# Performance work log

Measured on AMD Instinct MI355X. Metric: run time of the kernel, lower is better.

## Reference

```python
import jax, jax.numpy as jnp
import numpy as np

DIM = 1024
HEADS = 16
HEAD_DIM = DIM // HEADS
B, N = 512, 65
EPS = 1e-5


def layernorm(x, w, b):
    # LayerNorm over last dim (head_dim), eps matching torch default
    mu = jnp.mean(x, axis=-1, keepdims=True)
    var = jnp.var(x, axis=-1, keepdims=True)
    return (x - mu) * jax.lax.rsqrt(var + EPS) * w + b


def setup_inputs() -> dict:
    key = jax.random.key(0)
    ks = jax.random.split(key, 8)
    s = 0.02
    return {
        "x": jax.random.normal(ks[0], (B, N, DIM), dtype=jnp.float32),
        "w_qkv": jax.random.normal(ks[1], (3 * DIM, DIM), dtype=jnp.float32) * s,
        "w_proj": jax.random.normal(ks[2], (DIM, DIM), dtype=jnp.float32) * s,
        "qn_w": jnp.ones((HEAD_DIM,), jnp.float32),
        "qn_b": jnp.zeros((HEAD_DIM,), jnp.float32),
        "kn_w": jnp.ones((HEAD_DIM,), jnp.float32),
        "kn_b": jnp.zeros((HEAD_DIM,), jnp.float32),
        "bias": jax.random.normal(ks[3], (HEADS, 65, 65), dtype=jnp.float32) * 0.1,
        "bias_scale": jnp.array(1.0, jnp.float32),
    }


def reference(x, w_qkv, w_proj, qn_w, qn_b, kn_w, kn_b, bias, bias_scale):
    Bsz, n, C = x.shape
    scale = HEAD_DIM ** -0.5
    qkv = jnp.einsum('bnc,dc->bnd', x, w_qkv)              # [B,N,3C]
    qkv = qkv.reshape(Bsz, n, 3, HEADS, HEAD_DIM)
    qkv = jnp.transpose(qkv, (2, 0, 3, 1, 4))              # [3,B,H,N,hd]
    q, k, v = qkv[0], qkv[1], qkv[2]
    q = layernorm(q, qn_w, qn_b) * scale
    k = layernorm(k, kn_w, kn_b)
    attn = jnp.einsum('bhnd,bhmd->bhnm', q, k)             # [B,H,N,N]
    attn = attn + (bias[:, :n, :n] * bias_scale)[None]
    attn = jax.nn.softmax(attn, axis=-1)
    out = jnp.einsum('bhnm,bhmd->bhnd', attn, v)           # [B,H,N,hd]
    out = jnp.transpose(out, (0, 2, 1, 3)).reshape(Bsz, n, C)
    return jnp.einsum('bnc,dc->bnd', out, w_proj)
```

## Files before the change

kernel.cpp:

```cpp
#include <hip/hip_runtime.h>
#include <stdint.h>

#define HEADS 16
#define BSZ 512
#define NTOK 65
#define MTOK (BSZ * NTOK)
#define NX  34078720UL
#define NQW 3145728UL
#define NPW 1048576UL

typedef __attribute__((ext_vector_type(8))) short bf16x8;
typedef __attribute__((ext_vector_type(4))) float f32x4;

__device__ __forceinline__ unsigned short f2bf(float f) {
  unsigned u = __float_as_uint(f);
  u += 0x7FFFu + ((u >> 16) & 1u);
  return (unsigned short)(u >> 16);
}

__global__ __launch_bounds__(256) void cast3_kernel(
    const float* __restrict__ x, const float* __restrict__ wq, const float* __restrict__ wp,
    unsigned short* __restrict__ xb, unsigned short* __restrict__ wqb, unsigned short* __restrict__ wpb) {
  size_t u = ((size_t)blockIdx.x * 256 + threadIdx.x) * 4;
  const float* src; unsigned short* dst; size_t off;
  if (u < NX)            { src = x;  dst = xb;  off = u; }
  else if (u < NX + NQW) { src = wq; dst = wqb; off = u - NX; }
  else                   { src = wp; dst = wpb; off = u - NX - NQW; }
  float4 v = *(const float4*)(src + off);
  ushort4 o;
  o.x = f2bf(v.x); o.y = f2bf(v.y); o.z = f2bf(v.z); o.w = f2bf(v.w);
  *(ushort4*)(dst + off) = o;
}

__global__ __launch_bounds__(512, 2) void gemm0_256_kernel(
    const unsigned short* __restrict__ A, const unsigned short* __restrict__ Bm,
    unsigned short* __restrict__ qws, unsigned short* __restrict__ kws,
    unsigned short* __restrict__ vws,
    const float* __restrict__ qn_w, const float* __restrict__ qn_b,
    const float* __restrict__ kn_w, const float* __restrict__ kn_b) {
  __shared__ unsigned short As0[256 * 64];
  __shared__ unsigned short Bs0[256 * 64];
  __shared__ unsigned short As1[256 * 64];
  __shared__ unsigned short Bs1[256 * 64];
  const int tid = threadIdx.x;
  const int wid = tid >> 6, lane = tid & 63;
  const int lrow = lane & 15, lk = lane >> 4;
  const int wm = wid >> 2, wn = wid & 3;

  const int orig = blockIdx.x;
  const int wg = (orig & 7) * 195 + (orig >> 3);
  const int bm = wg / 12, bn = wg - bm * 12;

  const size_t arow0 = (size_t)bm * 256, brow0 = (size_t)bn * 256;

  const unsigned short* pA[4];
  const unsigned short* pB[4];
  int dstc[4];
#pragma unroll
  for (int j = 0; j < 4; ++j) {
    int ci = j * 512 + tid;
    int row = ci >> 3;
    int k8 = (ci & 7) ^ (row & 7);
    pA[j] = A + (arow0 + row) * 1024 + k8 * 8;
    pB[j] = Bm + (brow0 + row) * 1024 + k8 * 8;
    dstc[j] = (j * 512 + wid * 64) * 4;
  }

  f32x4 acc[2][4][4] = {};

  auto stage = [&](unsigned short* __restrict__ dA, unsigned short* __restrict__ dB, int ktn) {
    const int koff = ktn * 64;
#pragma unroll
    for (int j = 0; j < 4; ++j) {
      __builtin_amdgcn_global_load_lds(
          (const __attribute__((address_space(1))) unsigned int*)(pA[j] + koff),
          (__attribute__((address_space(3))) unsigned int*)dA + dstc[j], 16, 0, 0);
      __builtin_amdgcn_global_load_lds(
          (const __attribute__((address_space(1))) unsigned int*)(pB[j] + koff),
          (__attribute__((address_space(3))) unsigned int*)dB + dstc[j], 16, 0, 0);
    }
  };

  auto ktile = [&](const unsigned short* __restrict__ RA, const unsigned short* __restrict__ RB,
                   unsigned short* __restrict__ WA, unsigned short* __restrict__ WB, int ktn) {
    if (ktn < 16) stage(WA, WB, ktn);
#pragma unroll
    for (int kk = 0; kk < 2; ++kk) {
      const int cpos8 = ((kk * 4 + lk) ^ (lrow & 7)) * 8;
      bf16x8 bv[4];
#pragma unroll
      for (int nt = 0; nt < 4; ++nt)
        bv[nt] = *(const bf16x8*)&RB[(wn * 64 + nt * 16 + lrow) * 64 + cpos8];
#pragma unroll
      for (int mh = 0; mh < 2; ++mh) {
        bf16x8 av[4];
#pragma unroll
        for (int mt = 0; mt < 4; ++mt)
          av[mt] = *(const bf16x8*)&RA[(wm * 128 + mh * 64 + mt * 16 + lrow) * 64 + cpos8];
        __builtin_amdgcn_s_barrier();
        __builtin_amdgcn_s_setprio(1);
#pragma unroll
        for (int mt = 0; mt < 4; ++mt)
#pragma unroll
          for (int nt = 0; nt < 4; ++nt)
            acc[mh][mt][nt] =
                __builtin_amdgcn_mfma_f32_16x16x32_bf16(av[mt], bv[nt], acc[mh][mt][nt], 0, 0, 0);
        __builtin_amdgcn_s_setprio(0);
      }
    }
    __syncthreads();
  };

  stage(As0, Bs0, 0);
  __syncthreads();

#pragma unroll 1
  for (int kt2 = 0; kt2 < 8; ++kt2) {
    ktile(As0, Bs0, As1, Bs1, 2 * kt2 + 1);
    ktile(As1, Bs1, As0, Bs0, 2 * kt2 + 2);
  }

  const int sec = bn >> 2;
  const int h0 = ((bn & 3) << 2) + wn;
  const float qsc = (sec == 0) ? 0.125f : 1.0f;
  float wv[4], bvv[4];
  if (sec < 2) {
    const float* wp_ = sec ? kn_w : qn_w;
    const float* bp_ = sec ? kn_b : qn_b;
#pragma unroll
    for (int nt = 0; nt < 4; ++nt) {
      wv[nt] = wp_[nt * 16 + lrow];
      bvv[nt] = bp_[nt * 16 + lrow];
    }
  }
  unsigned short* qk_dst = sec ? kws : qws;
#pragma unroll
  for (int mh = 0; mh < 2; ++mh)
#pragma unroll
    for (int mt = 0; mt < 4; ++mt)
#pragma unroll
      for (int r = 0; r < 4; ++r) {
        int grow = bm * 256 + wm * 128 + mh * 64 + mt * 16 + lk * 4 + r;
        int b = grow / 65, nn = grow - b * 65;
        int bh = b * HEADS + h0;
        if (sec < 2) {
          float s = 0.f, s2 = 0.f;
#pragma unroll
          for (int nt = 0; nt < 4; ++nt) {
            float f = acc[mh][mt][nt][r];
            s += f; s2 += f * f;
          }
          s += __shfl_xor(s, 1); s2 += __shfl_xor(s2, 1);
          s += __shfl_xor(s, 2); s2 += __shfl_xor(s2, 2);
          s += __shfl_xor(s, 4); s2 += __shfl_xor(s2, 4);
          s += __shfl_xor(s, 8); s2 += __shfl_xor(s2, 8);
          float mu = s * 0.015625f;
          float rstd = rsqrtf(s2 * 0.015625f - mu * mu + 1e-5f);
          size_t base = ((size_t)bh * 65 + nn) * 64;
#pragma unroll
          for (int nt = 0; nt < 4; ++nt)
            qk_dst[base + nt * 16 + lrow] =
                f2bf(((acc[mh][mt][nt][r] - mu) * rstd * wv[nt] + bvv[nt]) * qsc);
        } else {
#pragma unroll
          for (int nt = 0; nt < 4; ++nt)
            vws[((size_t)bh * 64 + nt * 16 + lrow) * 80 + nn] = f2bf(acc[mh][mt][nt][r]);
        }
      }
}

template <int MODE>
__global__ __launch_bounds__(256) void gemm_bt_kernel(
    const unsigned short* __restrict__ A, const unsigned short* __restrict__ Bm,
    unsigned short* __restrict__ qws, unsigned short* __restrict__ kws,
    unsigned short* __restrict__ vws, float* __restrict__ outp,
    const float* __restrict__ qn_w, const float* __restrict__ qn_b,
    const float* __restrict__ kn_w, const float* __restrict__ kn_b) {
  __shared__ unsigned short As[128 * 64];
  __shared__ unsigned short Bs[128 * 64];
  const int tid = threadIdx.x;
  const int wid = tid >> 6, lane = tid & 63;
  const int lrow = lane & 15, lk = lane >> 4;
  const int bm = blockIdx.y, bn = blockIdx.x;
  const int wr = (wid >> 1) * 64, wc = (wid & 1) * 64;
  const size_t arow0 = (size_t)bm * 128, brow0 = (size_t)bn * 128;

  f32x4 acc[4][4] = {};

  for (int kt = 0; kt < 16; ++kt) {
    __syncthreads();
    const int k0 = kt * 64;
#pragma unroll
    for (int j = 0; j < 4; ++j) {
      int ci = j * 256 + tid;
      int row = ci >> 3, k8s = ci & 7;
      int k8 = k8s ^ (row & 7);
      const unsigned short* srcA = A + (arow0 + row) * 1024 + k0 + k8 * 8;
      __builtin_amdgcn_global_load_lds(
          (const __attribute__((address_space(1))) unsigned int*)srcA,
          (__attribute__((address_space(3))) unsigned int*)As + (size_t)(j * 256 + wid * 64) * 4,
          16, 0, 0);
      const unsigned short* srcB = Bm + (brow0 + row) * 1024 + k0 + k8 * 8;
      __builtin_amdgcn_global_load_lds(
          (const __attribute__((address_space(1))) unsigned int*)srcB,
          (__attribute__((address_space(3))) unsigned int*)Bs + (size_t)(j * 256 + wid * 64) * 4,
          16, 0, 0);
    }
    __syncthreads();
#pragma unroll
    for (int kk = 0; kk < 2; ++kk) {
      const int cpos = (kk * 4 + lk) ^ (lrow & 7);
      bf16x8 af[4], bfv[4];
#pragma unroll
      for (int mt = 0; mt < 4; ++mt)
        af[mt] = *(const bf16x8*)&As[(wr + mt * 16 + lrow) * 64 + cpos * 8];
#pragma unroll
      for (int nt = 0; nt < 4; ++nt)
        bfv[nt] = *(const bf16x8*)&Bs[(wc + nt * 16 + lrow) * 64 + cpos * 8];
#pragma unroll
      for (int mt = 0; mt < 4; ++mt)
#pragma unroll
        for (int nt = 0; nt < 4; ++nt)
          acc[mt][nt] = __builtin_amdgcn_mfma_f32_16x16x32_bf16(af[mt], bfv[nt], acc[mt][nt], 0, 0, 0);
    }
  }

  if (MODE == 0) {
  } else {
    const size_t cb = (size_t)bn * 128 + wc + lrow;
#pragma unroll
    for (int mt = 0; mt < 4; ++mt)
#pragma unroll
      for (int r = 0; r < 4; ++r) {
        float* rp = outp + (size_t)(bm * 128 + wr + mt * 16 + lk * 4 + r) * 1024 + cb;
#pragma unroll
        for (int nt = 0; nt < 4; ++nt) rp[nt * 16] = acc[mt][nt][r];
      }
  }
}

__global__ __launch_bounds__(256, 4) void attn_kernel(
    const unsigned short* __restrict__ qws, const unsigned short* __restrict__ kws,
    const unsigned short* __restrict__ vws,
    const float* __restrict__ bias, const float* __restrict__ bias_scale,
    unsigned short* __restrict__ aws) {
  __shared__ unsigned short qk_s[2 * 80 * 64];
  __shared__ unsigned short v_s[64 * 128];
  const int tid = threadIdx.x;
  const int wid = tid >> 6;
  const int bh = blockIdx.x;
  const int b = bh >> 4, h = bh & 15;
  const size_t qbase = (size_t)bh * 65 * 64;
  const size_t vbase = (size_t)bh * 64 * 80;

#pragma unroll
  for (int it = 0; it < 2; ++it) {
    int ci = it * 256 + tid;
    int row = ci >> 3, k8s = ci & 7;
    int k8 = k8s ^ (row & 7);
    __builtin_amdgcn_global_load_lds(
        (const __attribute__((address_space(1))) unsigned int*)(qws + qbase + row * 64 + k8 * 8),
        (__attribute__((address_space(3))) unsigned int*)qk_s + (size_t)(it * 256 + wid * 64) * 4,
        16, 0, 0);
    __builtin_amdgcn_global_load_lds(
        (const __attribute__((address_space(1))) unsigned int*)(kws + qbase + row * 64 + k8 * 8),
        (__attribute__((address_space(3))) unsigned int*)qk_s + (size_t)(640 + it * 256 + wid * 64) * 4,
        16, 0, 0);
  }
  if (tid < 8) {
    bf16x8 tq = *(const bf16x8*)&qws[qbase + 64 * 64 + tid * 8];
    *(bf16x8*)&qk_s[64 * 64 + tid * 8] = tq;
  } else if (tid < 16) {
    int t = tid - 8;
    bf16x8 tk = *(const bf16x8*)&kws[qbase + 64 * 64 + t * 8];
    *(bf16x8*)&qk_s[5120 + 64 * 64 + t * 8] = tk;
  }
#pragma unroll
  for (int it = 0; it < 4; ++it) {
    int ci = it * 256 + tid;
    int d = ci >> 4, cs = ci & 15;
    int c = cs ^ (d & 7);
    __builtin_amdgcn_global_load_lds(
        (const __attribute__((address_space(1))) unsigned int*)(vws + vbase + d * 80 + c * 8),
        (__attribute__((address_space(3))) unsigned int*)v_s + (size_t)(it * 256 + wid * 64) * 4,
        16, 0, 0);
  }
  __syncthreads();

  const int lane = tid & 63;
  const int lrow = lane & 15, lk = lane >> 4;
  const float bsc = *bias_scale;
  const unsigned short* q_s = qk_s;
  const unsigned short* k_s = qk_s + 5120;
  unsigned short* p_s = qk_s;

  auto qkt_softmax = [&](int s, unsigned int (&pk)[5][2]) {
    f32x4 accs[5] = {};
#pragma unroll
    for (int kk = 0; kk < 2; ++kk) {
      const int cpos = (kk * 4 + lk) ^ (lrow & 7);
      bf16x8 af = *(const bf16x8*)&q_s[(s * 16 + lrow) * 64 + cpos * 8];
#pragma unroll
      for (int nt = 0; nt < 5; ++nt) {
        bf16x8 bv = *(const bf16x8*)&k_s[(nt * 16 + lrow) * 64 + cpos * 8];
        accs[nt] = __builtin_amdgcn_mfma_f32_16x16x32_bf16(af, bv, accs[nt], 0, 0, 0);
      }
    }
#pragma unroll
    for (int r = 0; r < 4; ++r) {
      int row = s * 16 + lk * 4 + r;
      int brow = row > 64 ? 64 : row;
      float vals[5];
#pragma unroll
      for (int nt = 0; nt < 5; ++nt) {
        int col = nt * 16 + lrow;
        float v = accs[nt][r];
        if (col < 65) v += bias[((size_t)h * 65 + brow) * 65 + col] * bsc;
        else v = -1e30f;
        vals[nt] = v;
      }
      float m = vals[0];
#pragma unroll
      for (int nt = 1; nt < 5; ++nt) m = fmaxf(m, vals[nt]);
      m = fmaxf(m, __shfl_xor(m, 1)); m = fmaxf(m, __shfl_xor(m, 2));
      m = fmaxf(m, __shfl_xor(m, 4)); m = fmaxf(m, __shfl_xor(m, 8));
      float ssum = 0.f;
#pragma unroll
      for (int nt = 0; nt < 5; ++nt) { vals[nt] = __expf(vals[nt] - m); ssum += vals[nt]; }
      ssum += __shfl_xor(ssum, 1); ssum += __shfl_xor(ssum, 2);
      ssum += __shfl_xor(ssum, 4); ssum += __shfl_xor(ssum, 8);
      float inv = 1.0f / ssum;
#pragma unroll
      for (int nt = 0; nt < 5; ++nt) {
        unsigned int u = (unsigned int)f2bf(vals[nt] * inv);
        if ((r & 1) == 0) pk[nt][r >> 1] = u;
        else pk[nt][r >> 1] |= u << 16;
      }
    }
  };

  auto pwrite = [&](int s, const unsigned int (&pk)[5][2]) {
#pragma unroll
    for (int r = 0; r < 4; ++r) {
      int row = s * 16 + lk * 4 + r;
#pragma unroll
      for (int nt = 0; nt < 5; ++nt) {
        int col = nt * 16 + lrow;
        p_s[row * 128 + ((col >> 3) ^ (row & 7)) * 8 + (col & 7)] =
            (unsigned short)(pk[nt][r >> 1] >> ((r & 1) * 16));
      }
#pragma unroll
      for (int nt = 5; nt < 8; ++nt) {
        int col = nt * 16 + lrow;
        p_s[row * 128 + ((col >> 3) ^ (row & 7)) * 8 + (col & 7)] = 0;
      }
    }
  };

  unsigned int pk0[5][2], pk1[5][2];
  qkt_softmax(wid, pk0);
  if (wid == 0) qkt_softmax(4, pk1);
  __syncthreads();
  pwrite(wid, pk0);
  if (wid == 0) pwrite(4, pk1);
  __syncthreads();

  const size_t obase = (size_t)b * 65 * 1024 + h * 64;
  for (int s = wid; s < 5; s += 4) {
    f32x4 acco[4] = {};
#pragma unroll
    for (int kk = 0; kk < 3; ++kk) {
      const int cpos = (kk * 4 + lk) ^ (lrow & 7);
      bf16x8 af = *(const bf16x8*)&p_s[(s * 16 + lrow) * 128 + cpos * 8];
#pragma unroll
      for (int nt = 0; nt < 4; ++nt) {
        bf16x8 bv = *(const bf16x8*)&v_s[(nt * 16 + lrow) * 128 + cpos * 8];
        acco[nt] = __builtin_amdgcn_mfma_f32_16x16x32_bf16(af, bv, acco[nt], 0, 0, 0);
      }
    }
#pragma unroll
    for (int r = 0; r < 4; ++r) {
      int row = s * 16 + lk * 4 + r;
      if (row < 65) {
#pragma unroll
        for (int nt = 0; nt < 4; ++nt)
          aws[obase + (size_t)row * 1024 + nt * 16 + lrow] = f2bf(acco[nt][r]);
      }
    }
  }
}

extern "C" void kernel_launch(void* const* d_in, const int* in_sizes, int n_in,
                              void* d_out, int out_size, void* d_ws, size_t ws_size,
                              hipStream_t stream) {
  const float* x     = (const float*)d_in[0];
  const float* wqkv  = (const float*)d_in[1];
  const float* wproj = (const float*)d_in[2];
  const float* qn_w  = (const float*)d_in[3];
  const float* qn_b  = (const float*)d_in[4];
  const float* kn_w  = (const float*)d_in[5];
  const float* kn_b  = (const float*)d_in[6];
  const float* bias  = (const float*)d_in[7];
  const float* bsc   = (const float*)d_in[8];
  float* out = (float*)d_out;

  unsigned short* xb  = (unsigned short*)d_ws;
  unsigned short* wqb = xb + NX;
  unsigned short* wpb = wqb + NQW;
  unsigned short* qws = wpb + NPW;
  unsigned short* kws = qws + 34078720UL;
  unsigned short* vws = kws + 34078720UL;
  unsigned short* aws = vws + 41943040UL;

  cast3_kernel<<<37376, 256, 0, stream>>>(x, wqkv, wproj, xb, wqb, wpb);
  gemm0_256_kernel<<<1560, 512, 0, stream>>>(xb, wqb, qws, kws, vws,
                                             qn_w, qn_b, kn_w, kn_b);
  attn_kernel<<<8192, 256, 0, stream>>>(qws, kws, vws, bias, bsc, aws);
  gemm_bt_kernel<1><<<dim3(8, 260), 256, 0, stream>>>(aws, wpb, nullptr, nullptr, nullptr, out,
                                                      nullptr, nullptr, nullptr, nullptr);
}
```

Measured before the change: 741.3 us.

## Restructure QKV GEMM mainloop into 4-stage 32-wide K pipeline

Replaces the double-buffered 64-wide K tiles in the QKV projection GEMM with a four-slot ring of 32-wide K tiles, prefetching two tiles ahead. Explicit vmcnt waits with a single barrier per step replace the per-ktile __syncthreads and the mid-loop barriers. The swizzle is changed to suit the 32-element rows. The aim is deeper load/compute overlap and fewer barriers, at the cost of more loop iterations, each with less MFMA work to hide latency.

After: 793.9 us. 7.1% more time.

```diff
diff --git a/kernel.cpp b/kernel.cpp
--- a/kernel.cpp
+++ b/kernel.cpp
@@ -38,10 +38,8 @@
     unsigned short* __restrict__ vws,
     const float* __restrict__ qn_w, const float* __restrict__ qn_b,
     const float* __restrict__ kn_w, const float* __restrict__ kn_b) {
-  __shared__ unsigned short As0[256 * 64];
-  __shared__ unsigned short Bs0[256 * 64];
-  __shared__ unsigned short As1[256 * 64];
-  __shared__ unsigned short Bs1[256 * 64];
+  __shared__ unsigned short As4[4 * 256 * 32];
+  __shared__ unsigned short Bs4[4 * 256 * 32];
   const int tid = threadIdx.x;
   const int wid = tid >> 6, lane = tid & 63;
   const int lrow = lane & 15, lk = lane >> 4;
@@ -53,14 +51,14 @@
 
   const size_t arow0 = (size_t)bm * 256, brow0 = (size_t)bn * 256;
 
-  const unsigned short* pA[4];
-  const unsigned short* pB[4];
-  int dstc[4];
-#pragma unroll
-  for (int j = 0; j < 4; ++j) {
+  const unsigned short* pA[2];
+  const unsigned short* pB[2];
+  int dstc[2];
+#pragma unroll
+  for (int j = 0; j < 2; ++j) {
     int ci = j * 512 + tid;
-    int row = ci >> 3;
-    int k8 = (ci & 7) ^ (row & 7);
+    int row = ci >> 2;
+    int k8 = (ci & 3) ^ ((row >> 1) & 3);
     pA[j] = A + (arow0 + row) * 1024 + k8 * 8;
     pB[j] = Bm + (brow0 + row) * 1024 + k8 * 8;
     dstc[j] = (j * 512 + wid * 64) * 4;
@@ -68,10 +66,12 @@
 
   f32x4 acc[2][4][4] = {};
 
-  auto stage = [&](unsigned short* __restrict__ dA, unsigned short* __restrict__ dB, int ktn) {
-    const int koff = ktn * 64;
-#pragma unroll
-    for (int j = 0; j < 4; ++j) {
+  auto stage = [&](int t) {
+    const int koff = t * 32;
+    unsigned short* dA = As4 + (t & 3) * 8192;
+    unsigned short* dB = Bs4 + (t & 3) * 8192;
+#pragma unroll
+    for (int j = 0; j < 2; ++j) {
       __builtin_amdgcn_global_load_lds(
           (const __attribute__((address_space(1))) unsigned int*)(pA[j] + koff),
           (__attribute__((address_space(3))) unsigned int*)dA + dstc[j], 16, 0, 0);
@@ -81,44 +81,50 @@
     }
   };
 
-  auto ktile = [&](const unsigned short* __restrict__ RA, const unsigned short* __restrict__ RB,
-                   unsigned short* __restrict__ WA, unsigned short* __restrict__ WB, int ktn) {
-    if (ktn < 16) stage(WA, WB, ktn);
-#pragma unroll
-    for (int kk = 0; kk < 2; ++kk) {
-      const int cpos8 = ((kk * 4 + lk) ^ (lrow & 7)) * 8;
-      bf16x8 bv[4];
-#pragma unroll
-      for (int nt = 0; nt < 4; ++nt)
-        bv[nt] = *(const bf16x8*)&RB[(wn * 64 + nt * 16 + lrow) * 64 + cpos8];
-#pragma unroll
-      for (int mh = 0; mh < 2; ++mh) {
-        bf16x8 av[4];
-#pragma unroll
-        for (int mt = 0; mt < 4; ++mt)
-          av[mt] = *(const bf16x8*)&RA[(wm * 128 + mh * 64 + mt * 16 + lrow) * 64 + cpos8];
-        __builtin_amdgcn_s_barrier();
-        __builtin_amdgcn_s_setprio(1);
-#pragma unroll
-        for (int mt = 0; mt < 4; ++mt)
-#pragma unroll
-          for (int nt = 0; nt < 4; ++nt)
-            acc[mh][mt][nt] =
-                __builtin_amdgcn_mfma_f32_16x16x32_bf16(av[mt], bv[nt], acc[mh][mt][nt], 0, 0, 0);
-        __builtin_amdgcn_s_setprio(0);
-      }
-    }
-    __syncthreads();
+  auto compute = [&](int t) {
+    const unsigned short* RA = As4 + (t & 3) * 8192;
+    const unsigned short* RB = Bs4 + (t & 3) * 8192;
+    bf16x8 bv[4];
+#pragma unroll
+    for (int nt = 0; nt < 4; ++nt) {
+      int row = wn * 64 + nt * 16 + lrow;
+      bv[nt] = *(const bf16x8*)&RB[row * 32 + (lk ^ ((row >> 1) & 3)) * 8];
+    }
+#pragma unroll
+    for (int mh = 0; mh < 2; ++mh) {
+      bf16x8 av[4];
+#pragma unroll
+      for (int mt = 0; mt < 4; ++mt) {
+        int row = wm * 128 + mh * 64 + mt * 16 + lrow;
+        av[mt] = *(const bf16x8*)&RA[row * 32 + (lk ^ ((row >> 1) & 3)) * 8];
+      }
+      __builtin_amdgcn_s_setprio(1);
+#pragma unroll
+      for (int mt = 0; mt < 4; ++mt)
+#pragma unroll
+        for (int nt = 0; nt < 4; ++nt)
+          acc[mh][mt][nt] =
+              __builtin_amdgcn_mfma_f32_16x16x32_bf16(av[mt], bv[nt], acc[mh][mt][nt], 0, 0, 0);
+      __builtin_amdgcn_s_setprio(0);
+    }
   };
 
-  stage(As0, Bs0, 0);
-  __syncthreads();
+  stage(0);
+  stage(1);
+  asm volatile("s_waitcnt vmcnt(4)" ::: "memory");
+  __builtin_amdgcn_s_barrier();
 
 #pragma unroll 1
-  for (int kt2 = 0; kt2 < 8; ++kt2) {
-    ktile(As0, Bs0, As1, Bs1, 2 * kt2 + 1);
-    ktile(As1, Bs1, As0, Bs0, 2 * kt2 + 2);
-  }
+  for (int t = 0; t < 30; ++t) {
+    stage(t + 2);
+    compute(t);
+    asm volatile("s_waitcnt vmcnt(4)" ::: "memory");
+    __builtin_amdgcn_s_barrier();
+  }
+  compute(30);
+  asm volatile("s_waitcnt vmcnt(0)" ::: "memory");
+  __builtin_amdgcn_s_barrier();
+  compute(31);
 
   const int sec = bn >> 2;
   const int h0 = ((bn & 3) << 2) + wn;
```
